# Kernel optimization log

Measured on AMD Instinct MI355X. Metric: run time of the kernel, lower is better.

Reference implementation:

```python
import jax, jax.numpy as jnp
import numpy as np

# arch config (matches init_kwargs)
T = 8
G = 16
D = 64
GG = G * G
THR = 0.5            # arch.object_threshold
Z_COS_MATCH_W = 5.0  # arch.z_cos_match_weight
ADJ_W = 1.0
PRES_W = 1.0
POOL_W = 1.0
OBJ_W = 10.0
FLOW_W = 1.0
FULL_OBJ = 200000.0  # arch.full_object_weight
FLOW_END = 100000.0  # arch.flow_cooling_end_step


def setup_inputs() -> dict:
    key = jax.random.key(0)
    k1, k2, k3 = jax.random.split(key, 3)
    B = 128
    return {
        "z_what": jax.random.normal(k1, (T * B, GG, D), dtype=jnp.float32),
        "z_pres_prob": jax.random.uniform(k2, (T * B, GG, 1), dtype=jnp.float32),
        "grid_flow": jax.random.uniform(k3, (T * B, GG, 1), dtype=jnp.float32),
        "global_step": 50000,
    }


def _maxpool3x3(x):
    # x: (N, C, G, G); torch MaxPool2d(3, stride=1, padding=1) pads with -inf
    return jax.lax.reduce_window(
        x, -jnp.inf, jax.lax.max,
        window_dimensions=(1, 1, 3, 3), window_strides=(1, 1, 1, 1),
        padding=[(0, 0), (0, 0), (1, 1), (1, 1)])


def reference(z_what, z_pres_prob, grid_flow, global_step):
    B = z_what.shape[0] // T
    zw = z_what.reshape(T, B, GG, D)
    zp = z_pres_prob.reshape(T, B, GG, 1)

    # ---- z_what_loss_grid_cell: adjacent squared deltas ----
    z_what_loss = jnp.sum((zw[1:] - zw[:-1]) ** 2)

    # ---- z_pres_loss_grid_cell ----
    sim = 1.0 - (zp[2:] - zp[:-2]) ** 2
    deltas = (zp[2:] - zp[1:-1]) ** 2 + (zp[:-2] - zp[1:-1]) ** 2
    z_pres_loss = jnp.sum(sim * deltas)

    # ---- z_what_consistency_pool (cosine_sim branch) ----
    w = jnp.abs(zw) * zp                                    # (T,B,GG,D)
    wi = w.transpose(0, 1, 3, 2).reshape(T * B, D, G, G)
    smoothed = _maxpool3x3(wi).reshape(T, B, D, GG).transpose(0, 1, 3, 2)
    dot = jnp.sum(smoothed[:-1] * w[1:], axis=-1)           # (T-1,B,GG)
    na = jnp.maximum(jnp.sqrt(jnp.sum(smoothed[:-1] ** 2, -1)), 1e-6)
    nb = jnp.maximum(jnp.sqrt(jnp.sum(w[1:] ** 2, -1)), 1e-6)
    cos_pool = dot / (na * nb)
    pw = zp[..., 0]
    pw = (pw[:-1] + pw[1:]) * 0.5                           # (T-1,B,GG)
    z_what_loss_pool = -jnp.sum(cos_pool * pw)

    # ---- z_what_consistency_objects (vectorized over objects) ----
    # For every active cell (t,b,i,j) at time t<T-1, compare its z_what (prior)
    # with z_what at t+1 over the 3x3 circular neighborhood, restricted to
    # neighbor cells whose z_pres > threshold. Loss per object:
    #   -z_cos_match_weight * max(sim) + sum(sim); skipped if no active neighbor.
    zpg = zp.reshape(T, B, G, G)
    zwg = zw.reshape(T, B, G, G, D)
    prior = zwg[:-1]                                        # (T-1,B,G,G,D)
    prior_n = jnp.maximum(jnp.sqrt(jnp.sum(prior ** 2, -1)), 1e-8)
    pres_prior = zpg[:-1] > THR                             # (T-1,B,G,G)
    sum_sim = jnp.zeros(prior.shape[:-1], dtype=prior.dtype)
    max_sim = jnp.full(prior.shape[:-1], -jnp.inf, dtype=prior.dtype)
    has_nb = jnp.zeros(prior.shape[:-1], dtype=bool)
    for di in (-1, 0, 1):
        for dj in (-1, 0, 1):
            nbw = jnp.roll(zwg[1:], (-di, -dj), axis=(2, 3))       # circular
            nbp = jnp.roll(zpg[1:], (-di, -dj), axis=(2, 3)) > THR
            dotn = jnp.sum(prior * nbw, axis=-1)
            nn = jnp.maximum(jnp.sqrt(jnp.sum(nbw ** 2, -1)), 1e-8)
            s = dotn / (prior_n * nn)
            sum_sim = sum_sim + jnp.where(nbp, s, 0.0)
            max_sim = jnp.maximum(max_sim, jnp.where(nbp, s, -jnp.inf))
            has_nb = has_nb | nbp
    valid = pres_prior & has_nb
    contrib = jnp.where(valid, -Z_COS_MATCH_W * max_sim + sum_sim, 0.0)
    z_what_loss_objects = jnp.sum(contrib)
    objects_detected = jnp.sum(pres_prior.astype(jnp.int32))

    # ---- compute_flow_loss ----
    zp_img = z_pres_prob.reshape(-1, 1, G, G)
    zp_max = _maxpool3x3(zp_img).reshape(-1, GG, 1)
    flow = grid_flow.reshape(-1, GG, 1)
    fmask = flow > 0.5
    flow_loss = jnp.sum(jnp.where(fmask, (zp_max - flow) ** 2, 0.0)) \
        + 100.0 * jnp.maximum(0.0, jnp.sum(zp_img) - jnp.sum(flow))

    # ---- total (Space base loss excluded; external submodule) ----
    scale_obj = min(1.0, float(global_step) / FULL_OBJ)
    scale_flow = max(0.0, 1.0 - float(global_step) / FLOW_END)
    loss = (z_what_loss * ADJ_W
            + z_pres_loss * PRES_W
            + z_what_loss_pool * POOL_W
            + z_what_loss_objects * scale_obj * OBJ_W
            + flow_loss * FLOW_W * scale_flow)
    return loss
```

## Files before the change

### kernel.cpp

```cpp
#include <hip/hip_runtime.h>
#include <math.h>

#define TT 8
#define BB 128
#define GG 256
#define DD 64
#define NCH 4
#define CF4 4
#define ST 5


__device__ inline float wred(float v) {
#pragma unroll
    for (int off = 32; off > 0; off >>= 1) v += __shfl_xor(v, off, 64);
    return v;
}
__device__ inline float dot4(float4 a, float4 b) {
    return a.x * b.x + a.y * b.y + a.z * b.z + a.w * b.w;
}
__device__ inline float4 fabs4(float4 a) {
    return make_float4(fabsf(a.x), fabsf(a.y), fabsf(a.z), fabsf(a.w));
}
__device__ inline float4 max4(float4 a, float4 b) {
    return make_float4(fmaxf(a.x, b.x), fmaxf(a.y, b.y), fmaxf(a.z, b.z), fmaxf(a.w, b.w));
}
__device__ inline float4 scale4(float4 a, float s) {
    return make_float4(a.x * s, a.y * s, a.z * s, a.w * s);
}
__device__ inline float4 sub4(float4 a, float4 b) {
    return make_float4(a.x - b.x, a.y - b.y, a.z - b.z, a.w - b.w);
}

__device__ inline float rowmax3(float v) {
    int iv = __float_as_int(v);
    int a = __builtin_amdgcn_update_dpp(iv, iv, 0x101, 0xF, 0xF, false);
    int c = __builtin_amdgcn_update_dpp(iv, iv, 0x111, 0xF, 0xF, false);
    return fmaxf(v, fmaxf(__int_as_float(a), __int_as_float(c)));
}
__device__ inline float4 rowmax3_4(float4 v) {
    return make_float4(rowmax3(v.x), rowmax3(v.y), rowmax3(v.z), rowmax3(v.w));
}

__global__ __launch_bounds__(256) void pair_kernel(const float* __restrict__ zw,
                                                   const float* __restrict__ zp,
                                                   const float* __restrict__ flow,
                                                   float* __restrict__ ws) {
    const int pairIdx = blockIdx.x;
    const int t = pairIdx >> 7;
    const int b = pairIdx & (BB - 1);
    const int tid = threadIdx.x;
    const int gi = tid >> 4, gj = tid & 15;

    __shared__ float4 shB[GG * ST];
    __shared__ float4 shM[GG * ST];
    __shared__ float pA[GG], pB[GG], nrmB[GG];
    __shared__ float bred[7][4];

    const float4* gA = (const float4*)zw + (size_t)(t * BB + b) * 1024;
    const float4* gB = gA + (size_t)BB * 1024;

    const float pAc = zp[(size_t)(t * BB + b) * GG + tid];
    const float pBc = zp[(size_t)((t + 1) * BB + b) * GG + tid];
    pA[tid] = pAc;
    pB[tid] = pBc;

    int nbc[9];
    unsigned inbM = 0;
    {
        int m = 0;
#pragma unroll
        for (int di = -1; di <= 1; di++) {
#pragma unroll
            for (int dj = -1; dj <= 1; dj++) {
                nbc[m] = (((gi + di) & 15) << 4) | ((gj + dj) & 15);
                if (((unsigned)(gi + di) < 16u) && ((unsigned)(gj + dj) < 16u))
                    inbM |= (1u << m);
                m++;
            }
        }
    }

    float zdiff = 0.f, sa = 0.f, sb = 0.f, poolDot = 0.f, poolN = 0.f;
    float dots[9] = {0.f, 0.f, 0.f, 0.f, 0.f, 0.f, 0.f, 0.f, 0.f};
    const int sbase = tid * ST;

#pragma unroll 1
    for (int c = 0; c < NCH; c++) {
        float4 aA[CF4], aB[CF4];
#pragma unroll
        for (int q = 0; q < CF4; q++) {
            aA[q] = gA[tid * 16 + c * 4 + q];
            aB[q] = gB[tid * 16 + c * 4 + q];
        }

        float4 rm[CF4];
#pragma unroll
        for (int q = 0; q < CF4; q++) {
            shB[sbase + q] = aB[q];
            rm[q] = rowmax3_4(scale4(fabs4(aA[q]), pAc));
            shM[sbase + q] = rm[q];
        }
#pragma unroll
        for (int q = 0; q < CF4; q++) {
            float4 d = sub4(aB[q], aA[q]);
            zdiff += dot4(d, d);
            sa += dot4(aA[q], aA[q]);
            sb += dot4(aB[q], aB[q]);
            dots[4] += dot4(aA[q], aB[q]);
        }
        __syncthreads();

#pragma unroll
        for (int k = 0; k < 9; k++) {
            if (k == 4) continue;
            int base = nbc[k] * ST;
#pragma unroll
            for (int q = 0; q < CF4; q++) dots[k] += dot4(aA[q], shB[base + q]);
        }
        if (gi > 0) {
            int base = (tid - 16) * ST;
#pragma unroll
            for (int q = 0; q < CF4; q++) rm[q] = max4(rm[q], shM[base + q]);
        }
        if (gi < 15) {
            int base = (tid + 16) * ST;
#pragma unroll
            for (int q = 0; q < CF4; q++) rm[q] = max4(rm[q], shM[base + q]);
        }
#pragma unroll
        for (int q = 0; q < CF4; q++) {
            poolDot += dot4(rm[q], fabs4(aB[q]));
            poolN += dot4(rm[q], rm[q]);
        }
        __syncthreads();
    }

    nrmB[tid] = sqrtf(sb);
    __syncthreads();

    float prior_n = fmaxf(sqrtf(sa), 1e-8f);
    float sum_sim = 0.f, max_sim = -1e30f;
    bool has = false;
#pragma unroll
    for (int k = 0; k < 9; k++) {
        float nn = fmaxf(nrmB[nbc[k]], 1e-8f);
        float s = dots[k] / (prior_n * nn);
        if (pB[nbc[k]] > 0.5f) {
            sum_sim += s;
            max_sim = fmaxf(max_sim, s);
            has = true;
        }
    }
    float obj = ((pAc > 0.5f) && has) ? (sum_sim - 5.0f * max_sim) : 0.f;

    float na_pool = fmaxf(sqrtf(poolN), 1e-6f);
    float nb_pool = fmaxf(pBc * sqrtf(sb), 1e-6f);
    float poolc = -(pBc * poolDot) / (na_pool * nb_pool) * 0.5f * (pAc + pBc);

    float mx = pAc;
#pragma unroll
    for (int k = 0; k < 9; k++)
        if (k != 4 && ((inbM >> k) & 1u)) mx = fmaxf(mx, pA[nbc[k]]);
    float f = flow[(size_t)(t * BB + b) * GG + tid];
    float fsq = 0.f;
    if (f > 0.5f) { float d = mx - f; fsq = d * d; }
    float szp = pAc, sflow = f;
    if (t == 6) {
        float mxB = pBc;
#pragma unroll
        for (int k = 0; k < 9; k++)
            if (k != 4 && ((inbM >> k) & 1u)) mxB = fmaxf(mxB, pB[nbc[k]]);
        float f7 = flow[(size_t)(7 * BB + b) * GG + tid];
        if (f7 > 0.5f) { float d = mxB - f7; fsq += d * d; }
        szp += pBc;
        sflow += f7;
    }

    float pres = 0.f;
    if (t <= 5) {
        float pC = zp[(size_t)((t + 2) * BB + b) * GG + tid];
        float s02 = pC - pAc;
        float sim = 1.f - s02 * s02;
        float d2 = pC - pBc, d0 = pAc - pBc;
        pres = sim * (d2 * d2 + d0 * d0);
    }

    float r[7] = {zdiff, pres, poolc, obj, fsq, szp, sflow};
    int w = tid >> 6, lane = tid & 63;
#pragma unroll
    for (int j = 0; j < 7; j++) {
        float rv = wred(r[j]);
        if (lane == 0) bred[j][w] = rv;
    }
    __syncthreads();
    if (tid < 7)
        ws[pairIdx * 8 + tid] = bred[tid][0] + bred[tid][1] + bred[tid][2] + bred[tid][3];
}

__global__ __launch_bounds__(256) void final_kernel(const float* __restrict__ ws,
                                                    const int* __restrict__ gs,
                                                    float* __restrict__ out) {
    const int tid = threadIdx.x;
    __shared__ float bred[7][4];
    float c[7] = {0.f, 0.f, 0.f, 0.f, 0.f, 0.f, 0.f};
    for (int p = tid; p < (TT - 1) * BB; p += 256) {
        const float* r = ws + p * 8;
#pragma unroll
        for (int j = 0; j < 7; j++) c[j] += r[j];
    }
    int w = tid >> 6, lane = tid & 63;
#pragma unroll
    for (int j = 0; j < 7; j++) {
        float rv = wred(c[j]);
        if (lane == 0) bred[j][w] = rv;
    }
    __syncthreads();
    if (tid == 0) {
        float s[7];
#pragma unroll
        for (int j = 0; j < 7; j++) s[j] = bred[j][0] + bred[j][1] + bred[j][2] + bred[j][3];
        float step = (float)gs[0];
        float scale_obj = fminf(1.f, step / 200000.f);
        float scale_flow = fmaxf(0.f, 1.f - step / 100000.f);
        float flow_loss = s[4] + 100.f * fmaxf(0.f, s[5] - s[6]);
        out[0] = s[0]
               + s[1]
               + s[2]
               + s[3] * scale_obj * 10.0f
               + flow_loss * scale_flow;
    }
}

extern "C" void kernel_launch(void* const* d_in, const int* in_sizes, int n_in,
                              void* d_out, int out_size, void* d_ws, size_t ws_size,
                              hipStream_t stream) {
    const float* zw = (const float*)d_in[0];
    const float* zp = (const float*)d_in[1];
    const float* fl = (const float*)d_in[2];
    const int* gs = (const int*)d_in[3];
    float* ws = (float*)d_ws;

    pair_kernel<<<(TT - 1) * BB, 256, 0, stream>>>(zw, zp, fl, ws);
    final_kernel<<<1, 256, 0, stream>>>(ws, gs, (float*)d_out);
}
```

Measured before the change: 127.8 us.

## Double-buffer chunk loads with direct global-to-LDS copies and a q-major LDS layout

Each chunk's B tile is copied straight from global memory into LDS with global_load_lds, and the next chunk's A and B loads are issued before the current chunk is computed. The shared buffers are double-buffered, so only one barrier per chunk is needed. The padded cell-major layout is replaced by a q-major layout, which gives consecutive threads consecutive float4 addresses. This doubles LDS use and relies on global_load_lds with 16-byte width. The per-thread destination addressing may not match the wave-uniform LDS base semantics of that instruction.

```diff
diff --git a/kernel.cpp b/kernel.cpp
--- a/kernel.cpp
+++ b/kernel.cpp
@@ -7,7 +7,8 @@
 #define DD 64
 #define NCH 4
 #define CF4 4
-#define ST 5
+
+#define SIDX(q, cell) (((q) << 8) + (cell))
 
 
 __device__ inline float wred(float v) {
@@ -29,6 +30,13 @@
 }
 __device__ inline float4 sub4(float4 a, float4 b) {
     return make_float4(a.x - b.x, a.y - b.y, a.z - b.z, a.w - b.w);
+}
+
+__device__ inline void glds16(const float4* gsrc, float4* lds_dst) {
+    __builtin_amdgcn_global_load_lds(
+        (const __attribute__((address_space(1))) unsigned int*)gsrc,
+        (__attribute__((address_space(3))) unsigned int*)lds_dst,
+        16, 0, 0);
 }
 
 __device__ inline float rowmax3(float v) {
@@ -51,8 +59,8 @@
     const int tid = threadIdx.x;
     const int gi = tid >> 4, gj = tid & 15;
 
-    __shared__ float4 shB[GG * ST];
-    __shared__ float4 shM[GG * ST];
+    __shared__ float4 shB[2][NCH * GG];
+    __shared__ float4 shM[2][NCH * GG];
     __shared__ float pA[GG], pB[GG], nrmB[GG];
     __shared__ float bred[7][4];
 
@@ -65,72 +73,83 @@
     pB[tid] = pBc;
 
     int nbc[9];
-    unsigned inbM = 0;
     {
         int m = 0;
 #pragma unroll
-        for (int di = -1; di <= 1; di++) {
-#pragma unroll
-            for (int dj = -1; dj <= 1; dj++) {
-                nbc[m] = (((gi + di) & 15) << 4) | ((gj + dj) & 15);
-                if (((unsigned)(gi + di) < 16u) && ((unsigned)(gj + dj) < 16u))
-                    inbM |= (1u << m);
-                m++;
-            }
-        }
+        for (int di = -1; di <= 1; di++)
+#pragma unroll
+            for (int dj = -1; dj <= 1; dj++)
+                nbc[m++] = (((gi + di) & 15) << 4) | ((gj + dj) & 15);
     }
 
     float zdiff = 0.f, sa = 0.f, sb = 0.f, poolDot = 0.f, poolN = 0.f;
     float dots[9] = {0.f, 0.f, 0.f, 0.f, 0.f, 0.f, 0.f, 0.f, 0.f};
-    const int sbase = tid * ST;
+
+    float4 aA[CF4];
+#pragma unroll
+    for (int q = 0; q < CF4; q++) glds16(&gB[tid * 16 + q], &shB[0][SIDX(q, tid)]);
+#pragma unroll
+    for (int q = 0; q < CF4; q++) aA[q] = gA[tid * 16 + q];
+#pragma unroll
+    for (int q = 0; q < CF4; q++)
+        shM[0][SIDX(q, tid)] = rowmax3_4(scale4(fabs4(aA[q]), pAc));
+    __syncthreads();
 
 #pragma unroll 1
     for (int c = 0; c < NCH; c++) {
-        float4 aA[CF4], aB[CF4];
+        const int cur = c & 1, nxt = cur ^ 1;
+
+        float4 pfA[CF4];
+        if (c < NCH - 1) {
+#pragma unroll
+            for (int q = 0; q < CF4; q++)
+                glds16(&gB[tid * 16 + (c + 1) * 4 + q], &shB[nxt][SIDX(q, tid)]);
+#pragma unroll
+            for (int q = 0; q < CF4; q++) pfA[q] = gA[tid * 16 + (c + 1) * 4 + q];
+        }
+
+        float4 ownB[CF4];
+#pragma unroll
+        for (int q = 0; q < CF4; q++) ownB[q] = shB[cur][SIDX(q, tid)];
 #pragma unroll
         for (int q = 0; q < CF4; q++) {
-            aA[q] = gA[tid * 16 + c * 4 + q];
-            aB[q] = gB[tid * 16 + c * 4 + q];
-        }
-
-        float4 rm[CF4];
-#pragma unroll
-        for (int q = 0; q < CF4; q++) {
-            shB[sbase + q] = aB[q];
-            rm[q] = rowmax3_4(scale4(fabs4(aA[q]), pAc));
-            shM[sbase + q] = rm[q];
-        }
-#pragma unroll
-        for (int q = 0; q < CF4; q++) {
-            float4 d = sub4(aB[q], aA[q]);
+            float4 d = sub4(ownB[q], aA[q]);
             zdiff += dot4(d, d);
             sa += dot4(aA[q], aA[q]);
-            sb += dot4(aB[q], aB[q]);
-            dots[4] += dot4(aA[q], aB[q]);
-        }
-        __syncthreads();
-
+            sb += dot4(ownB[q], ownB[q]);
+            dots[4] += dot4(aA[q], ownB[q]);
+        }
 #pragma unroll
         for (int k = 0; k < 9; k++) {
             if (k == 4) continue;
-            int base = nbc[k] * ST;
-#pragma unroll
-            for (int q = 0; q < CF4; q++) dots[k] += dot4(aA[q], shB[base + q]);
-        }
-        if (gi > 0) {
-            int base = (tid - 16) * ST;
-#pragma unroll
-            for (int q = 0; q < CF4; q++) rm[q] = max4(rm[q], shM[base + q]);
-        }
-        if (gi < 15) {
-            int base = (tid + 16) * ST;
-#pragma unroll
-            for (int q = 0; q < CF4; q++) rm[q] = max4(rm[q], shM[base + q]);
-        }
-#pragma unroll
-        for (int q = 0; q < CF4; q++) {
-            poolDot += dot4(rm[q], fabs4(aB[q]));
-            poolN += dot4(rm[q], rm[q]);
+#pragma unroll
+            for (int q = 0; q < CF4; q++)
+                dots[k] += dot4(aA[q], shB[cur][SIDX(q, nbc[k])]);
+        }
+        {
+            float4 sm[CF4];
+#pragma unroll
+            for (int q = 0; q < CF4; q++) sm[q] = shM[cur][SIDX(q, tid)];
+            if (gi > 0) {
+#pragma unroll
+                for (int q = 0; q < CF4; q++) sm[q] = max4(sm[q], shM[cur][SIDX(q, tid - 16)]);
+            }
+            if (gi < 15) {
+#pragma unroll
+                for (int q = 0; q < CF4; q++) sm[q] = max4(sm[q], shM[cur][SIDX(q, tid + 16)]);
+            }
+#pragma unroll
+            for (int q = 0; q < CF4; q++) {
+                poolDot += dot4(sm[q], fabs4(ownB[q]));
+                poolN += dot4(sm[q], sm[q]);
+            }
+        }
+        if (c < NCH - 1) {
+#pragma unroll
+            for (int q = 0; q < CF4; q++)
+                shM[nxt][SIDX(q, tid)] = rowmax3_4(scale4(fabs4(pfA[q]), pAc));
+#pragma unroll
+            for (int q = 0; q < CF4; q++) aA[q] = pfA[q];
         }
         __syncthreads();
     }
@@ -159,8 +178,14 @@
 
     float mx = pAc;
 #pragma unroll
-    for (int k = 0; k < 9; k++)
-        if (k != 4 && ((inbM >> k) & 1u)) mx = fmaxf(mx, pA[nbc[k]]);
+    for (int di = -1; di <= 1; di++)
+#pragma unroll
+        for (int dj = -1; dj <= 1; dj++) {
+            if (di == 0 && dj == 0) continue;
+            int ni = gi + di, nj = gj + dj;
+            if (((unsigned)ni < 16u) && ((unsigned)nj < 16u))
+                mx = fmaxf(mx, pA[(ni << 4) + nj]);
+        }
     float f = flow[(size_t)(t * BB + b) * GG + tid];
     float fsq = 0.f;
     if (f > 0.5f) { float d = mx - f; fsq = d * d; }
@@ -168,8 +193,14 @@
     if (t == 6) {
         float mxB = pBc;
 #pragma unroll
-        for (int k = 0; k < 9; k++)
-            if (k != 4 && ((inbM >> k) & 1u)) mxB = fmaxf(mxB, pB[nbc[k]]);
+        for (int di = -1; di <= 1; di++)
+#pragma unroll
+            for (int dj = -1; dj <= 1; dj++) {
+                if (di == 0 && dj == 0) continue;
+                int ni = gi + di, nj = gj + dj;
+                if (((unsigned)ni < 16u) && ((unsigned)nj < 16u))
+                    mxB = fmaxf(mxB, pB[(ni << 4) + nj]);
+            }
         float f7 = flow[(size_t)(7 * BB + b) * GG + tid];
         if (f7 > 0.5f) { float d = mxB - f7; fsq += d * d; }
         szp += pBc;
```

Measured after the change: 152.3 us. +19.2%, slower.
